# Performance work log

Measured on AMD Instinct MI355X. Metric: run time of the kernel, lower is better.

The kernel has to match this reference:

```python
import jax, jax.numpy as jnp
import numpy as np

D_MODEL = 512
N_HEADS = 8
D_K = D_MODEL // N_HEADS
WINDOW = 64
SCALE = 1.0 / np.sqrt(D_K)


def setup_inputs() -> dict:
    key = jax.random.key(0)
    ks = jax.random.split(key, 9)
    B, S = 1, 2048
    s = 1.0 / np.sqrt(D_MODEL)
    inp = {
        "x": jax.random.normal(ks[0], (B, S, D_MODEL), dtype=jnp.float32),
        "Wq": jax.random.normal(ks[1], (D_MODEL, D_MODEL), dtype=jnp.float32) * s,
        "bq": jnp.zeros((D_MODEL,), dtype=jnp.float32),
        "Wk": jax.random.normal(ks[2], (D_MODEL, D_MODEL), dtype=jnp.float32) * s,
        "bk": jnp.zeros((D_MODEL,), dtype=jnp.float32),
        "Wv": jax.random.normal(ks[3], (D_MODEL, D_MODEL), dtype=jnp.float32) * s,
        "bv": jnp.zeros((D_MODEL,), dtype=jnp.float32),
        "Wo": jax.random.normal(ks[4], (D_MODEL, D_MODEL), dtype=jnp.float32) * s,
        "bo": jnp.zeros((D_MODEL,), dtype=jnp.float32),
    }
    return inp


def reference(x, Wq, bq, Wk, bk, Wv, bv, Wo, bo):
    B, S, _ = x.shape
    # projections (torch Linear: x @ W.T + b); split heads -> [B,S,H,dk]
    q = (x @ Wq.T + bq).reshape(B, S, N_HEADS, D_K)
    k = (x @ Wk.T + bk).reshape(B, S, N_HEADS, D_K)
    v = (x @ Wv.T + bv).reshape(B, S, N_HEADS, D_K)

    # banded window indices: position i attends to [i-W, i+W]
    L = 2 * WINDOW + 1
    offsets = jnp.arange(L) - WINDOW                    # [L]
    pos = jnp.arange(S)[:, None] + offsets[None, :]     # [S, L]
    valid = (pos >= 0) & (pos < S)                      # [S, L]
    posc = jnp.clip(pos, 0, S - 1)

    k_w = k[:, posc]                                    # [B, S, L, H, dk]
    v_w = v[:, posc]                                    # [B, S, L, H, dk]

    scores = jnp.einsum("bshd,bslhd->bhsl", q, k_w) * SCALE
    scores = jnp.where(valid[None, None, :, :], scores, -jnp.inf)
    attn = jax.nn.softmax(scores, axis=-1)              # [B, H, S, L]
    out = jnp.einsum("bhsl,bslhd->bshd", attn, v_w)     # [B, S, H, dk]
    out = out.reshape(B, S, D_MODEL)
    return out @ Wo.T + bo
```

## Files before the change

### kernel.cpp

```cpp
#include <hip/hip_runtime.h>
#include <hip/hip_bf16.h>
#include <math.h>

#define S_LEN  2048
#define DMODEL 512
#define NHEADS 8
#define DK     64
#define WIN    64

static constexpr float SCALE = 0.125f;

typedef short bf16x8 __attribute__((ext_vector_type(8)));
typedef float f32x4  __attribute__((ext_vector_type(4)));

__device__ __forceinline__ short bfh(float v)
{
    __hip_bfloat16 b = __float2bfloat16(v);
    return *reinterpret_cast<short*>(&b);
}
__device__ __forceinline__ float bf2f(short s)
{
    __hip_bfloat16 b = *reinterpret_cast<__hip_bfloat16*>(&s);
    return __bfloat162float(b);
}
__device__ __forceinline__ void split1(float v, short& h, short& l)
{
    h = bfh(v);
    l = bfh(v - bf2f(h));
}
__device__ __forceinline__ void split4(const float4 v, short4* hp, short4* lp)
{
    short4 h, l;
    split1(v.x, h.x, l.x);
    split1(v.y, h.y, l.y);
    split1(v.z, h.z, l.z);
    split1(v.w, h.w, l.w);
    *hp = h;
    *lp = l;
}

__global__ __launch_bounds__(256)
void cast_split5(const float* __restrict__ x,  const float* __restrict__ wq,
                 const float* __restrict__ wk, const float* __restrict__ wv,
                 const float* __restrict__ wo,
                 short* __restrict__ xh,  short* __restrict__ xl,
                 short* __restrict__ wqh, short* __restrict__ wql,
                 short* __restrict__ wkh, short* __restrict__ wkl,
                 short* __restrict__ wvh, short* __restrict__ wvl,
                 short* __restrict__ woh, short* __restrict__ wol)
{
    const float* s; short* h; short* l; int n4;
    switch (blockIdx.z) {
        case 0:  s = x;  h = xh;  l = xl;  n4 = 262144; break;
        case 1:  s = wq; h = wqh; l = wql; n4 = 65536;  break;
        case 2:  s = wk; h = wkh; l = wkl; n4 = 65536;  break;
        case 3:  s = wv; h = wvh; l = wvl; n4 = 65536;  break;
        default: s = wo; h = woh; l = wol; n4 = 65536;  break;
    }
    for (int i = blockIdx.x * 256 + threadIdx.x; i < n4; i += gridDim.x * 256) {
        const float4 v = ((const float4*)s)[i];
        split4(v, &((short4*)h)[i], &((short4*)l)[i]);
    }
}

template<int BM, int BN, int MT, int NT>
__device__ __forceinline__ void mfma_gemm_body(
    const short* __restrict__ Ahg, const short* __restrict__ Alg,
    const short* __restrict__ Bhg, const short* __restrict__ Blg,
    const float* __restrict__ bias, float* __restrict__ C,
    int row0, int col0)
{
    constexpr int KS = 40;
    __shared__ __align__(16) short Ah[BM * KS];
    __shared__ __align__(16) short Al[BM * KS];
    __shared__ __align__(16) short Bh[BN * KS];
    __shared__ __align__(16) short Bl[BN * KS];

    const int tid  = threadIdx.x;
    const int lane = tid & 63;
    const int wv   = tid >> 6;
    const int wm0  = (wv >> 1) * (MT * 16);
    const int wn0  = (wv & 1) * (NT * 16);
    const int col  = lane & 15;
    const int quad = lane >> 4;

    f32x4 acc[MT][NT];
#pragma unroll
    for (int i = 0; i < MT; ++i)
#pragma unroll
        for (int j = 0; j < NT; ++j)
            acc[i][j] = (f32x4)0.0f;

    for (int k0 = 0; k0 < 512; k0 += 32) {
        __syncthreads();
        for (int u = tid; u < BM * 4; u += 256) {
            const int r = u >> 2, c = u & 3;
            *(float4*)&Ah[r * KS + c * 8] =
                *(const float4*)(Ahg + (size_t)(row0 + r) * 512 + k0 + c * 8);
            *(float4*)&Al[r * KS + c * 8] =
                *(const float4*)(Alg + (size_t)(row0 + r) * 512 + k0 + c * 8);
        }
        for (int u = tid; u < BN * 4; u += 256) {
            const int r = u >> 2, c = u & 3;
            *(float4*)&Bh[r * KS + c * 8] =
                *(const float4*)(Bhg + (size_t)(col0 + r) * 512 + k0 + c * 8);
            *(float4*)&Bl[r * KS + c * 8] =
                *(const float4*)(Blg + (size_t)(col0 + r) * 512 + k0 + c * 8);
        }
        __syncthreads();

        bf16x8 af_h[MT], af_l[MT], bf_h[NT], bf_l[NT];
#pragma unroll
        for (int i = 0; i < MT; ++i) {
            const int m = wm0 + i * 16 + col;
            af_h[i] = *(const bf16x8*)&Ah[m * KS + quad * 8];
            af_l[i] = *(const bf16x8*)&Al[m * KS + quad * 8];
        }
#pragma unroll
        for (int j = 0; j < NT; ++j) {
            const int n = wn0 + j * 16 + col;
            bf_h[j] = *(const bf16x8*)&Bh[n * KS + quad * 8];
            bf_l[j] = *(const bf16x8*)&Bl[n * KS + quad * 8];
        }
#pragma unroll
        for (int i = 0; i < MT; ++i)
#pragma unroll
            for (int j = 0; j < NT; ++j) {
                acc[i][j] = __builtin_amdgcn_mfma_f32_16x16x32_bf16(af_h[i], bf_h[j], acc[i][j], 0, 0, 0);
                acc[i][j] = __builtin_amdgcn_mfma_f32_16x16x32_bf16(af_h[i], bf_l[j], acc[i][j], 0, 0, 0);
                acc[i][j] = __builtin_amdgcn_mfma_f32_16x16x32_bf16(af_l[i], bf_h[j], acc[i][j], 0, 0, 0);
            }
    }

#pragma unroll
    for (int j = 0; j < NT; ++j) {
        const int cc = col0 + wn0 + j * 16 + col;
        const float bv = bias[cc];
#pragma unroll
        for (int i = 0; i < MT; ++i) {
            const int rbase = row0 + wm0 + i * 16 + quad * 4;
#pragma unroll
            for (int e = 0; e < 4; ++e)
                C[(size_t)(rbase + e) * 512 + cc] = acc[i][j][e] + bv;
        }
    }
}

__global__ __launch_bounds__(256)
void gemm_qkv_mfma(const short* __restrict__ xh, const short* __restrict__ xl,
                   const short* __restrict__ wqh, const short* __restrict__ wql,
                   const short* __restrict__ wkh, const short* __restrict__ wkl,
                   const short* __restrict__ wvh, const short* __restrict__ wvl,
                   const float* __restrict__ bq, const float* __restrict__ bk,
                   const float* __restrict__ bv,
                   float* __restrict__ Qb, float* __restrict__ Kb, float* __restrict__ Vb)
{
    const short *wh, *wl; const float* b; float* C;
    if (blockIdx.z == 0)      { wh = wqh; wl = wql; b = bq; C = Qb; }
    else if (blockIdx.z == 1) { wh = wkh; wl = wkl; b = bk; C = Kb; }
    else                      { wh = wvh; wl = wvl; b = bv; C = Vb; }
    mfma_gemm_body<64, 64, 2, 2>(xh, xl, wh, wl, b, C,
                                 blockIdx.y * 64, blockIdx.x * 64);
}

__global__ __launch_bounds__(256)
void gemm_out_mfma(const short* __restrict__ ah, const short* __restrict__ al,
                   const short* __restrict__ wh, const short* __restrict__ wl,
                   const float* __restrict__ b, float* __restrict__ C)
{
    mfma_gemm_body<32, 64, 1, 2>(ah, al, wh, wl, b, C,
                                 blockIdx.y * 32, blockIdx.x * 64);
}

__global__ __launch_bounds__(256)
void banded_attn_mfma(const float* __restrict__ Q,
                      const float* __restrict__ K,
                      const float* __restrict__ V,
                      short* __restrict__ abh, short* __restrict__ abl)
{
    __shared__ __align__(16) short smem[64 * 200 + 192 * 72 + 2 * 32 * 72];
    __shared__ float pmax[4][32];
    __shared__ float psum[4][32];
    short* VtS = smem;
    short* KS  = smem + 64 * 200;
    short* QhS = KS + 192 * 72;
    short* QlS = QhS + 32 * 72;
    short* PhS = KS;
    short* PlS = KS + 32 * 200;

    const int h    = blockIdx.x;
    const int t0   = blockIdx.y * 32;
    const int tid  = threadIdx.x;
    const int lane = tid & 63;
    const int wv   = tid >> 6;
    const int col  = lane & 15;
    const int quad = lane >> 4;

    for (int u = tid; u < 32 * 16; u += 256) {
        const int r = u >> 4, c = u & 15;
        const float4 v = *(const float4*)(Q + (size_t)(t0 + r) * 512 + h * 64 + c * 4);
        short4 hh, ll;
        split4(v, &hh, &ll);
        *(short4*)&QhS[r * 72 + c * 4] = hh;
        *(short4*)&QlS[r * 72 + c * 4] = ll;
    }
    for (int u = tid; u < 192 * 16; u += 256) {
        const int r = u >> 4, c = u & 15;
        const int pos = t0 - 64 + r;
        float4 v = {0.f, 0.f, 0.f, 0.f};
        if (pos >= 0 && pos < S_LEN)
            v = *(const float4*)(K + (size_t)pos * 512 + h * 64 + c * 4);
        short4 kk;
        kk.x = bfh(v.x); kk.y = bfh(v.y); kk.z = bfh(v.z); kk.w = bfh(v.w);
        *(short4*)&KS[r * 72 + c * 4] = kk;
    }
#pragma unroll
    for (int ch = 0; ch < 3; ++ch) {
        const int pr  = ch * 64 + lane;
        const int pos = t0 - 64 + pr;
        const bool ok = (pos >= 0) && (pos < S_LEN);
#pragma unroll
        for (int c = 0; c < 4; ++c) {
            const int d0 = wv * 16 + c * 4;
            float4 v = {0.f, 0.f, 0.f, 0.f};
            if (ok) v = *(const float4*)(V + (size_t)pos * 512 + h * 64 + d0);
            VtS[(d0 + 0) * 200 + pr] = bfh(v.x);
            VtS[(d0 + 1) * 200 + pr] = bfh(v.y);
            VtS[(d0 + 2) * 200 + pr] = bfh(v.z);
            VtS[(d0 + 3) * 200 + pr] = bfh(v.w);
        }
    }
    __syncthreads();

    f32x4 sacc[2][3];
#pragma unroll
    for (int mi = 0; mi < 2; ++mi)
#pragma unroll
        for (int nj = 0; nj < 3; ++nj)
            sacc[mi][nj] = (f32x4)0.0f;

#pragma unroll
    for (int ks = 0; ks < 2; ++ks) {
        bf16x8 aqh[2], aql[2];
#pragma unroll
        for (int mi = 0; mi < 2; ++mi) {
            aqh[mi] = *(const bf16x8*)&QhS[(mi * 16 + col) * 72 + ks * 32 + quad * 8];
            aql[mi] = *(const bf16x8*)&QlS[(mi * 16 + col) * 72 + ks * 32 + quad * 8];
        }
#pragma unroll
        for (int nj = 0; nj < 3; ++nj) {
            const bf16x8 bk = *(const bf16x8*)&KS[(wv * 48 + nj * 16 + col) * 72 + ks * 32 + quad * 8];
#pragma unroll
            for (int mi = 0; mi < 2; ++mi) {
                sacc[mi][nj] = __builtin_amdgcn_mfma_f32_16x16x32_bf16(aqh[mi], bk, sacc[mi][nj], 0, 0, 0);
                sacc[mi][nj] = __builtin_amdgcn_mfma_f32_16x16x32_bf16(aql[mi], bk, sacc[mi][nj], 0, 0, 0);
            }
        }
    }

    float pv[2][3][4];
#pragma unroll
    for (int mi = 0; mi < 2; ++mi)
#pragma unroll
        for (int nj = 0; nj < 3; ++nj)
#pragma unroll
            for (int e = 0; e < 4; ++e) {
                const int r32 = mi * 16 + quad * 4 + e;
                const int n   = wv * 48 + nj * 16 + col;
                const int pos = t0 - 64 + n;
                const int d   = n - r32;
                const bool valid = (pos >= 0) && (pos < S_LEN) && (d >= 0) && (d <= 128);
                pv[mi][nj][e] = valid ? sacc[mi][nj][e] * SCALE : -__builtin_inff();
            }

#pragma unroll
    for (int mi = 0; mi < 2; ++mi)
#pragma unroll
        for (int e = 0; e < 4; ++e) {
            float mx = fmaxf(fmaxf(pv[mi][0][e], pv[mi][1][e]), pv[mi][2][e]);
#pragma unroll
            for (int off = 1; off < 16; off <<= 1)
                mx = fmaxf(mx, __shfl_xor(mx, off));
            if ((lane & 15) == 0) pmax[wv][mi * 16 + quad * 4 + e] = mx;
        }
    __syncthreads();

#pragma unroll
    for (int mi = 0; mi < 2; ++mi)
#pragma unroll
        for (int e = 0; e < 4; ++e) {
            const int r32 = mi * 16 + quad * 4 + e;
            const float m = fmaxf(fmaxf(pmax[0][r32], pmax[1][r32]),
                                  fmaxf(pmax[2][r32], pmax[3][r32]));
            float ss = 0.f;
#pragma unroll
            for (int nj = 0; nj < 3; ++nj) {
                const float p = __expf(pv[mi][nj][e] - m);
                pv[mi][nj][e] = p;
                ss += p;
            }
#pragma unroll
            for (int off = 1; off < 16; off <<= 1)
                ss += __shfl_xor(ss, off);
            if ((lane & 15) == 0) psum[wv][r32] = ss;
#pragma unroll
            for (int nj = 0; nj < 3; ++nj) {
                const int n = wv * 48 + nj * 16 + col;
                const float p = pv[mi][nj][e];
                const short ph = bfh(p);
                PhS[r32 * 200 + n] = ph;
                PlS[r32 * 200 + n] = bfh(p - bf2f(ph));
            }
        }
    __syncthreads();

    const int mi = wv >> 1;
    f32x4 oacc[2];
    oacc[0] = (f32x4)0.0f;
    oacc[1] = (f32x4)0.0f;
#pragma unroll
    for (int ks = 0; ks < 6; ++ks) {
        const bf16x8 pah = *(const bf16x8*)&PhS[(mi * 16 + col) * 200 + ks * 32 + quad * 8];
        const bf16x8 pal = *(const bf16x8*)&PlS[(mi * 16 + col) * 200 + ks * 32 + quad * 8];
#pragma unroll
        for (int t = 0; t < 2; ++t) {
            const int nj = (wv & 1) * 2 + t;
            const bf16x8 vb = *(const bf16x8*)&VtS[(nj * 16 + col) * 200 + ks * 32 + quad * 8];
            oacc[t] = __builtin_amdgcn_mfma_f32_16x16x32_bf16(pah, vb, oacc[t], 0, 0, 0);
            oacc[t] = __builtin_amdgcn_mfma_f32_16x16x32_bf16(pal, vb, oacc[t], 0, 0, 0);
        }
    }

    float linv[4];
#pragma unroll
    for (int e = 0; e < 4; ++e) {
        const int r32 = mi * 16 + quad * 4 + e;
        const float l = psum[0][r32] + psum[1][r32] + psum[2][r32] + psum[3][r32];
        linv[e] = 1.0f / l;
    }
#pragma unroll
    for (int t = 0; t < 2; ++t) {
        const int nj = (wv & 1) * 2 + t;
#pragma unroll
        for (int e = 0; e < 4; ++e) {
            const int r32 = mi * 16 + quad * 4 + e;
            const float val = oacc[t][e] * linv[e];
            short hh, ll;
            split1(val, hh, ll);
            const size_t idx = (size_t)(t0 + r32) * 512 + h * 64 + nj * 16 + col;
            abh[idx] = hh;
            abl[idx] = ll;
        }
    }
}

extern "C" void kernel_launch(void* const* d_in, const int* in_sizes, int n_in,
                              void* d_out, int out_size, void* d_ws, size_t ws_size,
                              hipStream_t stream)
{
    const float* x  = (const float*)d_in[0];
    const float* Wq = (const float*)d_in[1];
    const float* bq = (const float*)d_in[2];
    const float* Wk = (const float*)d_in[3];
    const float* bk = (const float*)d_in[4];
    const float* Wv = (const float*)d_in[5];
    const float* bv = (const float*)d_in[6];
    const float* Wo = (const float*)d_in[7];
    const float* bo = (const float*)d_in[8];
    float* out = (float*)d_out;

    char* ws = (char*)d_ws;
    float* Qb = (float*)(ws);
    float* Kb = (float*)(ws + (4u << 20));
    float* Vb = (float*)(ws + (8u << 20));
    short* xh = (short*)(ws + (16u << 20));
    short* xl = (short*)(ws + (18u << 20));
    short* wqh = (short*)(ws + (20u << 20));
    short* wql = (short*)(ws + (20u << 20) + (512u << 10));
    short* wkh = (short*)(ws + (21u << 20));
    short* wkl = (short*)(ws + (21u << 20) + (512u << 10));
    short* wvh = (short*)(ws + (22u << 20));
    short* wvl = (short*)(ws + (22u << 20) + (512u << 10));
    short* woh = (short*)(ws + (23u << 20));
    short* wol = (short*)(ws + (23u << 20) + (512u << 10));
    short* abh = xh;
    short* abl = xl;

    dim3 gc(256, 1, 5);
    cast_split5<<<gc, 256, 0, stream>>>(x, Wq, Wk, Wv, Wo,
                                        xh, xl, wqh, wql, wkh, wkl,
                                        wvh, wvl, woh, wol);

    dim3 gq(DMODEL / 64, S_LEN / 64, 3);
    gemm_qkv_mfma<<<gq, 256, 0, stream>>>(xh, xl, wqh, wql, wkh, wkl, wvh, wvl,
                                          bq, bk, bv, Qb, Kb, Vb);

    dim3 ga(NHEADS, S_LEN / 32);
    banded_attn_mfma<<<ga, 256, 0, stream>>>(Qb, Kb, Vb, abh, abl);

    dim3 go(DMODEL / 64, S_LEN / 32);
    gemm_out_mfma<<<go, 256, 0, stream>>>(abh, abl, woh, wol, bo, out);
}
```

Baseline: 125.0 us.

## Drop low-order bf16 splits, emit bf16 QKV, use LDS DMA with swizzle

```diff
diff --git a/kernel.cpp b/kernel.cpp
--- a/kernel.cpp
+++ b/kernel.cpp
@@ -28,165 +28,210 @@
     h = bfh(v);
     l = bfh(v - bf2f(h));
 }
-__device__ __forceinline__ void split4(const float4 v, short4* hp, short4* lp)
-{
-    short4 h, l;
-    split1(v.x, h.x, l.x);
-    split1(v.y, h.y, l.y);
-    split1(v.z, h.z, l.z);
-    split1(v.w, h.w, l.w);
-    *hp = h;
-    *lp = l;
+
+__device__ __forceinline__ void dma16(const void* g, void* l)
+{
+    __builtin_amdgcn_global_load_lds(
+        (const __attribute__((address_space(1))) unsigned int*)g,
+        (__attribute__((address_space(3))) unsigned int*)l, 16, 0, 0);
 }
 
 __global__ __launch_bounds__(256)
-void cast_split5(const float* __restrict__ x,  const float* __restrict__ wq,
-                 const float* __restrict__ wk, const float* __restrict__ wv,
-                 const float* __restrict__ wo,
-                 short* __restrict__ xh,  short* __restrict__ xl,
-                 short* __restrict__ wqh, short* __restrict__ wql,
-                 short* __restrict__ wkh, short* __restrict__ wkl,
-                 short* __restrict__ wvh, short* __restrict__ wvl,
-                 short* __restrict__ woh, short* __restrict__ wol)
-{
-    const float* s; short* h; short* l; int n4;
-    switch (blockIdx.z) {
-        case 0:  s = x;  h = xh;  l = xl;  n4 = 262144; break;
-        case 1:  s = wq; h = wqh; l = wql; n4 = 65536;  break;
-        case 2:  s = wk; h = wkh; l = wkl; n4 = 65536;  break;
-        case 3:  s = wv; h = wvh; l = wvl; n4 = 65536;  break;
-        default: s = wo; h = woh; l = wol; n4 = 65536;  break;
-    }
-    for (int i = blockIdx.x * 256 + threadIdx.x; i < n4; i += gridDim.x * 256) {
-        const float4 v = ((const float4*)s)[i];
-        split4(v, &((short4*)h)[i], &((short4*)l)[i]);
+void cast_ws(const float* __restrict__ x,  const float* __restrict__ wq,
+             const float* __restrict__ wk, const float* __restrict__ wv,
+             const float* __restrict__ wo,
+             short* __restrict__ xh, short* __restrict__ xl,
+             short* __restrict__ wqb, short* __restrict__ wkb,
+             short* __restrict__ wvb, short* __restrict__ wob)
+{
+    const int z = blockIdx.z;
+    if (z == 0) {
+        for (int i = blockIdx.x * 256 + threadIdx.x; i < 262144; i += gridDim.x * 256) {
+            const float4 v = ((const float4*)x)[i];
+            short4 h, l;
+            split1(v.x, h.x, l.x);
+            split1(v.y, h.y, l.y);
+            split1(v.z, h.z, l.z);
+            split1(v.w, h.w, l.w);
+            ((short4*)xh)[i] = h;
+            ((short4*)xl)[i] = l;
+        }
+    } else {
+        const float* s; short* d;
+        switch (z) {
+            case 1:  s = wq; d = wqb; break;
+            case 2:  s = wk; d = wkb; break;
+            case 3:  s = wv; d = wvb; break;
+            default: s = wo; d = wob; break;
+        }
+        for (int i = blockIdx.x * 256 + threadIdx.x; i < 65536; i += gridDim.x * 256) {
+            const float4 v = ((const float4*)s)[i];
+            short4 o;
+            o.x = bfh(v.x); o.y = bfh(v.y); o.z = bfh(v.z); o.w = bfh(v.w);
+            ((short4*)d)[i] = o;
+        }
     }
 }
 
 template<int BM, int BN, int MT, int NT>
-__device__ __forceinline__ void mfma_gemm_body(
-    const short* __restrict__ Ahg, const short* __restrict__ Alg,
-    const short* __restrict__ Bhg, const short* __restrict__ Blg,
-    const float* __restrict__ bias, float* __restrict__ C,
-    int row0, int col0)
-{
-    constexpr int KS = 40;
-    __shared__ __align__(16) short Ah[BM * KS];
-    __shared__ __align__(16) short Al[BM * KS];
-    __shared__ __align__(16) short Bh[BN * KS];
-    __shared__ __align__(16) short Bl[BN * KS];
+__device__ __forceinline__ void gemm2_acc(const short* __restrict__ Ahg,
+                                          const short* __restrict__ Alg,
+                                          const short* __restrict__ Bg,
+                                          int row0, int col0,
+                                          f32x4 acc[MT][NT])
+{
+    __shared__ __align__(16) short sAh[BM * 32];
+    __shared__ __align__(16) short sAl[BM * 32];
+    __shared__ __align__(16) short sB [BN * 32];
 
     const int tid  = threadIdx.x;
     const int lane = tid & 63;
     const int wv   = tid >> 6;
+    const int col  = lane & 15;
+    const int quad = lane >> 4;
     const int wm0  = (wv >> 1) * (MT * 16);
     const int wn0  = (wv & 1) * (NT * 16);
+    const int lr   = lane >> 2;
+    const int lc   = lane & 3;
+    constexpr int nIss = (2 * BM + BN) / 16;
+
+#pragma unroll
+    for (int i = 0; i < MT; ++i)
+#pragma unroll
+        for (int j = 0; j < NT; ++j)
+            acc[i][j] = (f32x4)0.0f;
+
+    for (int k0 = 0; k0 < 512; k0 += 32) {
+        __syncthreads();
+        for (int i = wv; i < nIss; i += 4) {
+            const short* src; short* dst; int grp, ro;
+            if (i < BM / 16)          { grp = i;            src = Ahg; dst = sAh; ro = row0; }
+            else if (i < BM / 8)      { grp = i - BM / 16;  src = Alg; dst = sAl; ro = row0; }
+            else                      { grp = i - BM / 8;   src = Bg;  dst = sB;  ro = col0; }
+            const int r  = grp * 16 + lr;
+            const int cs = lc ^ ((r >> 1) & 3);
+            dma16(src + (size_t)(ro + r) * 512 + k0 + cs * 8, dst + grp * 512);
+        }
+        __syncthreads();
+
+        bf16x8 fh[MT], fl[MT], fb[NT];
+#pragma unroll
+        for (int mi = 0; mi < MT; ++mi) {
+            const int m = wm0 + mi * 16 + col;
+            const int p = quad ^ ((m >> 1) & 3);
+            fh[mi] = *(const bf16x8*)&sAh[m * 32 + p * 8];
+            fl[mi] = *(const bf16x8*)&sAl[m * 32 + p * 8];
+        }
+#pragma unroll
+        for (int nj = 0; nj < NT; ++nj) {
+            const int n = wn0 + nj * 16 + col;
+            const int p = quad ^ ((n >> 1) & 3);
+            fb[nj] = *(const bf16x8*)&sB[n * 32 + p * 8];
+        }
+#pragma unroll
+        for (int mi = 0; mi < MT; ++mi)
+#pragma unroll
+            for (int nj = 0; nj < NT; ++nj) {
+                acc[mi][nj] = __builtin_amdgcn_mfma_f32_16x16x32_bf16(fh[mi], fb[nj], acc[mi][nj], 0, 0, 0);
+                acc[mi][nj] = __builtin_amdgcn_mfma_f32_16x16x32_bf16(fl[mi], fb[nj], acc[mi][nj], 0, 0, 0);
+            }
+    }
+}
+
+__global__ __launch_bounds__(256)
+void gemm_qkv2(const short* __restrict__ xh, const short* __restrict__ xl,
+               const short* __restrict__ wqb, const short* __restrict__ wkb,
+               const short* __restrict__ wvb,
+               const float* __restrict__ bq, const float* __restrict__ bk,
+               const float* __restrict__ bv,
+               short* __restrict__ qh, short* __restrict__ ql,
+               short* __restrict__ kb, short* __restrict__ vb)
+{
+    const int z = blockIdx.z;
+    const short* B; const float* bias;
+    if (z == 0)      { B = wqb; bias = bq; }
+    else if (z == 1) { B = wkb; bias = bk; }
+    else             { B = wvb; bias = bv; }
+    const int row0 = blockIdx.y * 64, col0 = blockIdx.x * 64;
+
+    f32x4 acc[2][2];
+    gemm2_acc<64, 64, 2, 2>(xh, xl, B, row0, col0, acc);
+
+    const int tid  = threadIdx.x;
+    const int lane = tid & 63;
+    const int wv   = tid >> 6;
     const int col  = lane & 15;
     const int quad = lane >> 4;
-
-    f32x4 acc[MT][NT];
-#pragma unroll
-    for (int i = 0; i < MT; ++i)
-#pragma unroll
-        for (int j = 0; j < NT; ++j)
-            acc[i][j] = (f32x4)0.0f;
-
-    for (int k0 = 0; k0 < 512; k0 += 32) {
-        __syncthreads();
-        for (int u = tid; u < BM * 4; u += 256) {
-            const int r = u >> 2, c = u & 3;
-            *(float4*)&Ah[r * KS + c * 8] =
-                *(const float4*)(Ahg + (size_t)(row0 + r) * 512 + k0 + c * 8);
-            *(float4*)&Al[r * KS + c * 8] =
-                *(const float4*)(Alg + (size_t)(row0 + r) * 512 + k0 + c * 8);
-        }
-        for (int u = tid; u < BN * 4; u += 256) {
-            const int r = u >> 2, c = u & 3;
-            *(float4*)&Bh[r * KS + c * 8] =
-                *(const float4*)(Bhg + (size_t)(col0 + r) * 512 + k0 + c * 8);
-            *(float4*)&Bl[r * KS + c * 8] =
-                *(const float4*)(Blg + (size_t)(col0 + r) * 512 + k0 + c * 8);
-        }
-        __syncthreads();
-
-        bf16x8 af_h[MT], af_l[MT], bf_h[NT], bf_l[NT];
-#pragma unroll
-        for (int i = 0; i < MT; ++i) {
-            const int m = wm0 + i * 16 + col;
-            af_h[i] = *(const bf16x8*)&Ah[m * KS + quad * 8];
-            af_l[i] = *(const bf16x8*)&Al[m * KS + quad * 8];
-        }
-#pragma unroll
-        for (int j = 0; j < NT; ++j) {
-            const int n = wn0 + j * 16 + col;
-            bf_h[j] = *(const bf16x8*)&Bh[n * KS + quad * 8];
-            bf_l[j] = *(const bf16x8*)&Bl[n * KS + quad * 8];
-        }
-#pragma unroll
-        for (int i = 0; i < MT; ++i)
-#pragma unroll
-            for (int j = 0; j < NT; ++j) {
-                acc[i][j] = __builtin_amdgcn_mfma_f32_16x16x32_bf16(af_h[i], bf_h[j], acc[i][j], 0, 0, 0);
-                acc[i][j] = __builtin_amdgcn_mfma_f32_16x16x32_bf16(af_h[i], bf_l[j], acc[i][j], 0, 0, 0);
-                acc[i][j] = __builtin_amdgcn_mfma_f32_16x16x32_bf16(af_l[i], bf_h[j], acc[i][j], 0, 0, 0);
-            }
-    }
-
-#pragma unroll
-    for (int j = 0; j < NT; ++j) {
-        const int cc = col0 + wn0 + j * 16 + col;
-        const float bv = bias[cc];
-#pragma unroll
-        for (int i = 0; i < MT; ++i) {
-            const int rbase = row0 + wm0 + i * 16 + quad * 4;
-#pragma unroll
-            for (int e = 0; e < 4; ++e)
-                C[(size_t)(rbase + e) * 512 + cc] = acc[i][j][e] + bv;
+    const int wm0  = (wv >> 1) * 32;
+    const int wn0  = (wv & 1) * 32;
+
+#pragma unroll
+    for (int nj = 0; nj < 2; ++nj) {
+        const int cc = col0 + wn0 + nj * 16 + col;
+        const float bias_v = bias[cc];
+#pragma unroll
+        for (int mi = 0; mi < 2; ++mi) {
+#pragma unroll
+            for (int e = 0; e < 4; ++e) {
+                const int row = row0 + wm0 + mi * 16 + quad * 4 + e;
+                const float val = acc[mi][nj][e] + bias_v;
+                const size_t idx = (size_t)row * 512 + cc;
+                if (z == 0) {
+                    short hh, ll;
+                    split1(val, hh, ll);
+                    qh[idx] = hh;
+                    ql[idx] = ll;
+                } else if (z == 1) {
+                    kb[idx] = bfh(val);
+                } else {
+                    vb[idx] = bfh(val);
+                }
+            }
         }
     }
 }
 
 __global__ __launch_bounds__(256)
-void gemm_qkv_mfma(const short* __restrict__ xh, const short* __restrict__ xl,
-                   const short* __restrict__ wqh, const short* __restrict__ wql,
-                   const short* __restrict__ wkh, const short* __restrict__ wkl,
-                   const short* __restrict__ wvh, const short* __restrict__ wvl,
-                   const float* __restrict__ bq, const float* __restrict__ bk,
-                   const float* __restrict__ bv,
-                   float* __restrict__ Qb, float* __restrict__ Kb, float* __restrict__ Vb)
-{
-    const short *wh, *wl; const float* b; float* C;
-    if (blockIdx.z == 0)      { wh = wqh; wl = wql; b = bq; C = Qb; }
-    else if (blockIdx.z == 1) { wh = wkh; wl = wkl; b = bk; C = Kb; }
-    else                      { wh = wvh; wl = wvl; b = bv; C = Vb; }
-    mfma_gemm_body<64, 64, 2, 2>(xh, xl, wh, wl, b, C,
-                                 blockIdx.y * 64, blockIdx.x * 64);
+void gemm_out2(const short* __restrict__ ah, const short* __restrict__ al,
+               const short* __restrict__ wob, const float* __restrict__ bo,
+               float* __restrict__ out)
+{
+    const int row0 = blockIdx.y * 32, col0 = blockIdx.x * 64;
+    f32x4 acc[1][2];
+    gemm2_acc<32, 64, 1, 2>(ah, al, wob, row0, col0, acc);
+
+    const int tid  = threadIdx.x;
+    const int lane = tid & 63;
+    const int wv   = tid >> 6;
+    const int col  = lane & 15;
+    const int quad = lane >> 4;
+    const int wm0  = (wv >> 1) * 16;
+    const int wn0  = (wv & 1) * 32;
+
+#pragma unroll
+    for (int nj = 0; nj < 2; ++nj) {
+        const int cc = col0 + wn0 + nj * 16 + col;
+        const float bias_v = bo[cc];
+#pragma unroll
+        for (int e = 0; e < 4; ++e) {
+            const int row = row0 + wm0 + quad * 4 + e;
+            out[(size_t)row * 512 + cc] = acc[0][nj][e] + bias_v;
+        }
+    }
 }
 
 __global__ __launch_bounds__(256)
-void gemm_out_mfma(const short* __restrict__ ah, const short* __restrict__ al,
-                   const short* __restrict__ wh, const short* __restrict__ wl,
-                   const float* __restrict__ b, float* __restrict__ C)
-{
-    mfma_gemm_body<32, 64, 1, 2>(ah, al, wh, wl, b, C,
-                                 blockIdx.y * 32, blockIdx.x * 64);
-}
-
-__global__ __launch_bounds__(256)
-void banded_attn_mfma(const float* __restrict__ Q,
-                      const float* __restrict__ K,
-                      const float* __restrict__ V,
-                      short* __restrict__ abh, short* __restrict__ abl)
-{
-    __shared__ __align__(16) short smem[64 * 200 + 192 * 72 + 2 * 32 * 72];
+void banded_attn2(const short* __restrict__ qh, const short* __restrict__ ql,
+                  const short* __restrict__ kb, const short* __restrict__ vb,
+                  short* __restrict__ abh, short* __restrict__ abl)
+{
+    __shared__ __align__(16) short VtS[64 * 200];
+    __shared__ __align__(16) short KS [192 * 64];
+    __shared__ __align__(16) short QhS[32 * 64];
+    __shared__ __align__(16) short QlS[32 * 64];
     __shared__ float pmax[4][32];
     __shared__ float psum[4][32];
-    short* VtS = smem;
-    short* KS  = smem + 64 * 200;
-    short* QhS = KS + 192 * 72;
-    short* QlS = QhS + 32 * 72;
-    short* PhS = KS;
-    short* PlS = KS + 32 * 200;
+    short* PS = KS;
 
     const int h    = blockIdx.x;
     const int t0   = blockIdx.y * 32;
@@ -196,38 +241,45 @@
     const int col  = lane & 15;
     const int quad = lane >> 4;
 
-    for (int u = tid; u < 32 * 16; u += 256) {
-        const int r = u >> 4, c = u & 15;
-        const float4 v = *(const float4*)(Q + (size_t)(t0 + r) * 512 + h * 64 + c * 4);
-        short4 hh, ll;
-        split4(v, &hh, &ll);
-        *(short4*)&QhS[r * 72 + c * 4] = hh;
-        *(short4*)&QlS[r * 72 + c * 4] = ll;
-    }
-    for (int u = tid; u < 192 * 16; u += 256) {
-        const int r = u >> 4, c = u & 15;
-        const int pos = t0 - 64 + r;
-        float4 v = {0.f, 0.f, 0.f, 0.f};
-        if (pos >= 0 && pos < S_LEN)
-            v = *(const float4*)(K + (size_t)pos * 512 + h * 64 + c * 4);
-        short4 kk;
-        kk.x = bfh(v.x); kk.y = bfh(v.y); kk.z = bfh(v.z); kk.w = bfh(v.w);
-        *(short4*)&KS[r * 72 + c * 4] = kk;
+    {
+        const int lr = lane >> 3;
+        const int lc = lane & 7;
+        for (int i = wv; i < 32; i += 4) {
+            const short* src; short* dst; int r;
+            if (i < 4) {
+                r = i * 8 + lr;
+                src = qh + (size_t)(t0 + r) * 512 + h * 64;
+                dst = QhS + i * 512;
+            } else if (i < 8) {
+                const int g = i - 4;
+                r = g * 8 + lr;
+                src = ql + (size_t)(t0 + r) * 512 + h * 64;
+                dst = QlS + g * 512;
+            } else {
+                const int g = i - 8;
+                r = g * 8 + lr;
+                int pos = t0 - 64 + r;
+                pos = pos < 0 ? 0 : (pos > 2047 ? 2047 : pos);
+                src = kb + (size_t)pos * 512 + h * 64;
+                dst = KS + g * 512;
+            }
+            const int cs = lc ^ (r & 7);
+            dma16(src + cs * 8, dst);
+        }
     }
 #pragma unroll
     for (int ch = 0; ch < 3; ++ch) {
         const int pr  = ch * 64 + lane;
-        const int pos = t0 - 64 + pr;
-        const bool ok = (pos >= 0) && (pos < S_LEN);
+        int pos = t0 - 64 + pr;
+        pos = pos < 0 ? 0 : (pos > 2047 ? 2047 : pos);
 #pragma unroll
         for (int c = 0; c < 4; ++c) {
             const int d0 = wv * 16 + c * 4;
-            float4 v = {0.f, 0.f, 0.f, 0.f};
-            if (ok) v = *(const float4*)(V + (size_t)pos * 512 + h * 64 + d0);
-            VtS[(d0 + 0) * 200 + pr] = bfh(v.x);
-            VtS[(d0 + 1) * 200 + pr] = bfh(v.y);
-            VtS[(d0 + 2) * 200 + pr] = bfh(v.z);
-            VtS[(d0 + 3) * 200 + pr] = bfh(v.w);
+            const short4 v = *(const short4*)(vb + (size_t)pos * 512 + h * 64 + d0);
+            VtS[(d0 + 0) * 200 + pr] = v.x;
+            VtS[(d0 + 1) * 200 + pr] = v.y;
+            VtS[(d0 + 2) * 200 + pr] = v.z;
+            VtS[(d0 + 3) * 200 + pr] = v.w;
         }
     }
     __syncthreads();
@@ -241,19 +293,24 @@
 
 #pragma unroll
     for (int ks = 0; ks < 2; ++ks) {
+        const int q0 = ks * 4 + quad;
         bf16x8 aqh[2], aql[2];
 #pragma unroll
         for (int mi = 0; mi < 2; ++mi) {
-            aqh[mi] = *(const bf16x8*)&QhS[(mi * 16 + col) * 72 + ks * 32 + quad * 8];
-            aql[mi] = *(const bf16x8*)&QlS[(mi * 16 + col) * 72 + ks * 32 + quad * 8];
+            const int m = mi * 16 + col;
+            const int p = q0 ^ (m & 7);
+            aqh[mi] = *(const bf16x8*)&QhS[m * 64 + p * 8];
+            aql[mi] = *(const bf16x8*)&QlS[m * 64 + p * 8];
         }
 #pragma unroll
         for (int nj = 0; nj < 3; ++nj) {
-            const bf16x8 bk = *(const bf16x8*)&KS[(wv * 48 + nj * 16 + col) * 72 + ks * 32 + quad * 8];
+            const int n = wv * 48 + nj * 16 + col;
+            const int p = q0 ^ (n & 7);
+            const bf16x8 bkf = *(const bf16x8*)&KS[n * 64 + p * 8];
 #pragma unroll
             for (int mi = 0; mi < 2; ++mi) {
-                sacc[mi][nj] = __builtin_amdgcn_mfma_f32_16x16x32_bf16(aqh[mi], bk, sacc[mi][nj], 0, 0, 0);
-                sacc[mi][nj] = __builtin_amdgcn_mfma_f32_16x16x32_bf16(aql[mi], bk, sacc[mi][nj], 0, 0, 0);
+                sacc[mi][nj] = __builtin_amdgcn_mfma_f32_16x16x32_bf16(aqh[mi], bkf, sacc[mi][nj], 0, 0, 0);
+                sacc[mi][nj] = __builtin_amdgcn_mfma_f32_16x16x32_bf16(aql[mi], bkf, sacc[mi][nj], 0, 0, 0);
             }
         }
     }
@@ -306,10 +363,7 @@
 #pragma unroll
             for (int nj = 0; nj < 3; ++nj) {
                 const int n = wv * 48 + nj * 16 + col;
-                const float p = pv[mi][nj][e];
-                const short ph = bfh(p);
-                PhS[r32 * 200 + n] = ph;
-                PlS[r32 * 200 + n] = bfh(p - bf2f(ph));
+                PS[r32 * 200 + n] = bfh(pv[mi][nj][e]);
             }
         }
     __syncthreads();
@@ -320,14 +374,12 @@
     oacc[1] = (f32x4)0.0f;
 #pragma unroll
     for (int ks = 0; ks < 6; ++ks) {
-        const bf16x8 pah = *(const bf16x8*)&PhS[(mi * 16 + col) * 200 + ks * 32 + quad * 8];
-        const bf16x8 pal = *(const bf16x8*)&PlS[(mi * 16 + col) * 200 + ks * 32 + quad * 8];
+        const bf16x8 pa = *(const bf16x8*)&PS[(mi * 16 + col) * 200 + ks * 32 + quad * 8];
 #pragma unroll
         for (int t = 0; t < 2; ++t) {
             const int nj = (wv & 1) * 2 + t;
-            const bf16x8 vb = *(const bf16x8*)&VtS[(nj * 16 + col) * 200 + ks * 32 + quad * 8];
-            oacc[t] = __builtin_amdgcn_mfma_f32_16x16x32_bf16(pah, vb, oacc[t], 0, 0, 0);
-            oacc[t] = __builtin_amdgcn_mfma_f32_16x16x32_bf16(pal, vb, oacc[t], 0, 0, 0);
+            const bf16x8 vf = *(const bf16x8*)&VtS[(nj * 16 + col) * 200 + ks * 32 + quad * 8];
+            oacc[t] = __builtin_amdgcn_mfma_f32_16x16x32_bf16(pa, vf, oacc[t], 0, 0, 0);
         }
     }
 
@@ -335,8 +387,7 @@
 #pragma unroll
     for (int e = 0; e < 4; ++e) {
         const int r32 = mi * 16 + quad * 4 + e;
-        const float l = psum[0][r32] + psum[1][r32] + psum[2][r32] + psum[3][r32];
-        linv[e] = 1.0f / l;
+        linv[e] = 1.0f / (psum[0][r32] + psum[1][r32] + psum[2][r32] + psum[3][r32]);
     }
 #pragma unroll
     for (int t = 0; t < 2; ++t) {
@@ -370,34 +421,30 @@
     float* out = (float*)d_out;
 
     char* ws = (char*)d_ws;
-    float* Qb = (float*)(ws);
-    float* Kb = (float*)(ws + (4u << 20));
-    float* Vb = (float*)(ws + (8u << 20));
-    short* xh = (short*)(ws + (16u << 20));
-    short* xl = (short*)(ws + (18u << 20));
-    short* wqh = (short*)(ws + (20u << 20));
-    short* wql = (short*)(ws + (20u << 20) + (512u << 10));
-    short* wkh = (short*)(ws + (21u << 20));
-    short* wkl = (short*)(ws + (21u << 20) + (512u << 10));
-    short* wvh = (short*)(ws + (22u << 20));
-    short* wvl = (short*)(ws + (22u << 20) + (512u << 10));
-    short* woh = (short*)(ws + (23u << 20));
-    short* wol = (short*)(ws + (23u << 20) + (512u << 10));
+    short* qh  = (short*)(ws);
+    short* ql  = (short*)(ws + (2u << 20));
+    short* kb  = (short*)(ws + (4u << 20));
+    short* vb  = (short*)(ws + (6u << 20));
+    short* xh  = (short*)(ws + (8u << 20));
+    short* xl  = (short*)(ws + (10u << 20));
+    short* wqb = (short*)(ws + (12u << 20));
+    short* wkb = (short*)(ws + (12u << 20) + 1 * (512u << 10));
+    short* wvb = (short*)(ws + (12u << 20) + 2 * (512u << 10));
+    short* wob = (short*)(ws + (12u << 20) + 3 * (512u << 10));
     short* abh = xh;
     short* abl = xl;
 
-    dim3 gc(256, 1, 5);
-    cast_split5<<<gc, 256, 0, stream>>>(x, Wq, Wk, Wv, Wo,
-                                        xh, xl, wqh, wql, wkh, wkl,
-                                        wvh, wvl, woh, wol);
+    dim3 gc(128, 1, 5);
+    cast_ws<<<gc, 256, 0, stream>>>(x, Wq, Wk, Wv, Wo,
+                                    xh, xl, wqb, wkb, wvb, wob);
 
     dim3 gq(DMODEL / 64, S_LEN / 64, 3);
-    gemm_qkv_mfma<<<gq, 256, 0, stream>>>(xh, xl, wqh, wql, wkh, wkl, wvh, wvl,
-                                          bq, bk, bv, Qb, Kb, Vb);
+    gemm_qkv2<<<gq, 256, 0, stream>>>(xh, xl, wqb, wkb, wvb,
+                                      bq, bk, bv, qh, ql, kb, vb);
 
     dim3 ga(NHEADS, S_LEN / 32);
-    banded_attn_mfma<<<ga, 256, 0, stream>>>(Qb, Kb, Vb, abh, abl);
+    banded_attn2<<<ga, 256, 0, stream>>>(qh, ql, kb, vb, abh, abl);
 
     dim3 go(DMODEL / 64, S_LEN / 32);
-    gemm_out_mfma<<<go, 256, 0, stream>>>(abh, abl, woh, wol, bo, out);
-}
+    gemm_out2<<<go, 256, 0, stream>>>(abh, abl, wob, bo, out);
+}
```

Measured after the change: 118.6 us. 1.05x faster.
